# Performance work log

Hardware: AMD Instinct MI355X
Metric: run time of the kernel (lower is better)

The kernel has to match this reference:

```python
import jax, jax.numpy as jnp
import numpy as np

B, S, D, H = 2, 512, 512, 8
HD = D // H  # 64


def setup_inputs() -> dict:
    key = jax.random.key(0)
    ks = jax.random.split(key, 14)
    sd = 1.0 / np.sqrt(D)
    sh = 1.0 / np.sqrt(HD)
    return {
        "query": jax.random.normal(ks[0], (B, S, D), jnp.float32),
        "key_": jax.random.normal(ks[1], (B, S, D), jnp.float32),
        "value": jax.random.normal(ks[2], (B, S, D), jnp.float32),
        "Wq": jax.random.uniform(ks[3], (D, D), jnp.float32, -sd, sd),
        "bq": jax.random.uniform(ks[4], (D,), jnp.float32, -sd, sd),
        "Wk": jax.random.uniform(ks[5], (D, D), jnp.float32, -sd, sd),
        "bk": jax.random.uniform(ks[6], (D,), jnp.float32, -sd, sd),
        "Wv": jax.random.uniform(ks[7], (D, D), jnp.float32, -sd, sd),
        "bv": jax.random.uniform(ks[8], (D,), jnp.float32, -sd, sd),
        "Wo": jax.random.uniform(ks[9], (D, D), jnp.float32, -sd, sd),
        "bo": jax.random.uniform(ks[10], (D,), jnp.float32, -sd, sd),
        "Aq": jax.random.uniform(ks[11], (HD, HD), jnp.float32, -sh, sh),
        "Ak": jax.random.uniform(ks[12], (HD, HD), jnp.float32, -sh, sh),
        "av": jax.random.normal(ks[13], (HD,), jnp.float32) * sh,
    }


def _heads(x):
    b, s, _ = x.shape
    return x.reshape(b, s, H, HD).transpose(0, 2, 1, 3)  # [b,h,s,hd]


def reference(query, key_, value, Wq, bq, Wk, bk, Wv, bv, Wo, bo, Aq, Ak, av):
    q = _heads(query @ Wq + bq)   # [b,h,q,hd]
    k = _heads(key_ @ Wk + bk)    # [b,h,k,hd]
    v = _heads(value @ Wv + bv)   # [b,h,k,hd]
    # additive (Bahdanau-style) scores: tanh(add_q(q)[:,:,:,None]+add_k(k)[:,:,None]) . av
    q_term = (q @ Aq)[:, :, :, None, :]   # [b,h,q,1,hd]
    k_term = (k @ Ak)[:, :, None, :, :]   # [b,h,1,k,hd]
    scores = jnp.einsum('bhqkd,d->bhqk', jnp.tanh(q_term + k_term), av)
    attn_weights = jax.nn.softmax(scores, axis=-1)  # dropout is identity at eval
    ctx = jnp.einsum('bhqk,bhkd->bhqd', attn_weights, v)
    b, _, s, _ = ctx.shape
    ctx = ctx.transpose(0, 2, 1, 3).reshape(b, s, D)
    out = ctx @ Wo + bo
    return out, attn_weights
```

## Files before the change

kernel.cpp:

```cpp
#include <hip/hip_runtime.h>
#include <math.h>

#define Bb 2
#define Ss 512
#define Dd 512
#define Hh 8
#define HDd 64
#define BS (Bb*Ss)

#if __has_builtin(__builtin_amdgcn_exp2f)
#define EXP2F(x) __builtin_amdgcn_exp2f(x)
#else
#define EXP2F(x) exp2f(x)
#endif
#if __has_builtin(__builtin_amdgcn_rcpf)
#define RCPF(x) __builtin_amdgcn_rcpf(x)
#else
#define RCPF(x) (1.0f/(x))
#endif

typedef float v4f __attribute__((ext_vector_type(4)));
typedef short v8s __attribute__((ext_vector_type(8)));

struct HL { short h, l; };

__device__ __forceinline__ HL split1(float x) {
  unsigned u = __builtin_bit_cast(unsigned, x);
  unsigned h = (u + 0x7fffu + ((u >> 16) & 1u)) >> 16;
  float hf = __builtin_bit_cast(float, h << 16);
  float lo = x - hf;
  unsigned ul = __builtin_bit_cast(unsigned, lo);
  unsigned l = (ul + 0x7fffu + ((ul >> 16) & 1u)) >> 16;
  HL r; r.h = (short)h; r.l = (short)l;
  return r;
}

__device__ __forceinline__ void split8p(const float* __restrict__ xp, v8s& ah, v8s& al) {
#pragma unroll
  for (int j = 0; j < 8; j++) {
    const HL r = split1(xp[j]);
    ah[j] = r.h; al[j] = r.l;
  }
}

__device__ __forceinline__ void split8v(float4 x0, float4 x1, v8s& ah, v8s& al) {
  HL r;
  r = split1(x0.x); ah[0] = r.h; al[0] = r.l;
  r = split1(x0.y); ah[1] = r.h; al[1] = r.l;
  r = split1(x0.z); ah[2] = r.h; al[2] = r.l;
  r = split1(x0.w); ah[3] = r.h; al[3] = r.l;
  r = split1(x1.x); ah[4] = r.h; al[4] = r.l;
  r = split1(x1.y); ah[5] = r.h; al[5] = r.l;
  r = split1(x1.z); ah[6] = r.h; al[6] = r.l;
  r = split1(x1.w); ah[7] = r.h; al[7] = r.l;
}

__global__ __launch_bounds__(256) void qkv_all(
    const float* __restrict__ Xq, const float* __restrict__ Xk, const float* __restrict__ Xv,
    const float* __restrict__ Wq, const float* __restrict__ Wk, const float* __restrict__ Wv,
    const float* __restrict__ Wo,
    const float* __restrict__ bq, const float* __restrict__ bk, const float* __restrict__ bv,
    const float* __restrict__ Aq, const float* __restrict__ Ak,
    float* __restrict__ EQ, float* __restrict__ EKt, float* __restrict__ Vw,
    short* __restrict__ WoPk)
{
  __shared__ __align__(16) short fragH[2][4][64][8];
  __shared__ __align__(16) short fragL[2][4][64][8];
  __shared__ float qs[64][68];
  __shared__ float qs2[16][260];

  const int z = blockIdx.z;
  const float* X    = (z == 0) ? Xq : (z == 1) ? Xk : Xv;
  const float* W    = (z == 0) ? Wq : (z == 1) ? Wk : Wv;
  const float* bias = (z == 0) ? bq : (z == 1) ? bk : bv;
  const int tid = threadIdx.x, l = tid & 63, w = tid >> 6;
  const int lm = l & 15, lq = l >> 4;
  const int h = blockIdx.x;
  const int r0 = blockIdx.y * 64;

  v4f acc[4] = {{0.f,0.f,0.f,0.f},{0.f,0.f,0.f,0.f},{0.f,0.f,0.f,0.f},{0.f,0.f,0.f,0.f}};
  const float* xrow = X + (size_t)(r0 + w * 16 + lm) * Dd + lq * 8;

  for (int kt = 0; kt < 16; ++kt) {
    const int buf = kt & 1;
    const float4 xa0 = *(const float4*)&xrow[kt * 32];
    const float4 xa1 = *(const float4*)&xrow[kt * 32 + 4];
    {
      v8s hh, ll;
#pragma unroll
      for (int j = 0; j < 8; j++) {
        const float x = W[(size_t)(kt * 32 + lq * 8 + j) * Dd + h * 64 + w * 16 + lm];
        const HL r = split1(x);
        hh[j] = r.h; ll[j] = r.l;
      }
      *(v8s*)&fragH[buf][w][l][0] = hh;
      *(v8s*)&fragL[buf][w][l][0] = ll;
    }
    __syncthreads();
    v8s ah, al;
    split8v(xa0, xa1, ah, al);
#pragma unroll
    for (int t = 0; t < 4; t++) {
      const v8s bh = *(const v8s*)&fragH[buf][t][l][0];
      const v8s bl = *(const v8s*)&fragL[buf][t][l][0];
      acc[t] = __builtin_amdgcn_mfma_f32_16x16x32_bf16(ah, bh, acc[t], 0, 0, 0);
      acc[t] = __builtin_amdgcn_mfma_f32_16x16x32_bf16(ah, bl, acc[t], 0, 0, 0);
      acc[t] = __builtin_amdgcn_mfma_f32_16x16x32_bf16(al, bh, acc[t], 0, 0, 0);
    }
  }

  if (z == 2) {
#pragma unroll
    for (int t = 0; t < 4; t++) {
      const int n = h * 64 + t * 16 + lm;
      const float bvv = bias[n];
#pragma unroll
      for (int r = 0; r < 4; r++)
        Vw[(size_t)(r0 + w * 16 + lq * 4 + r) * Dd + n] = acc[t][r] + bvv;
    }
    {
      const int tau = (blockIdx.y * 8 + h) * 4 + w;
      const int nt = tau >> 4, kt = tau & 15;
      v8s hh, ll;
#pragma unroll
      for (int j = 0; j < 8; j++) {
        const float x = Wo[(size_t)(kt * 32 + lq * 8 + j) * Dd + nt * 16 + lm];
        const HL r = split1(x);
        hh[j] = r.h; ll[j] = r.l;
      }
      *(v8s*)&WoPk[((size_t)tau * 64 + l) * 16 + 0] = hh;
      *(v8s*)&WoPk[((size_t)tau * 64 + l) * 16 + 8] = ll;
    }
    return;
  }

#pragma unroll
  for (int t = 0; t < 4; t++) {
    const int n = h * 64 + t * 16 + lm;
    const float bvv = bias[n];
#pragma unroll
    for (int r = 0; r < 4; r++)
      qs[w * 16 + lq * 4 + r][t * 16 + lm] = acc[t][r] + bvv;
  }
  __syncthreads();

  const float* Am = (z == 0) ? Aq : Ak;
  v4f a2[4] = {{0.f,0.f,0.f,0.f},{0.f,0.f,0.f,0.f},{0.f,0.f,0.f,0.f},{0.f,0.f,0.f,0.f}};
#pragma unroll
  for (int kt2 = 0; kt2 < 2; ++kt2) {
    v8s ah, al;
    split8p(&qs[w * 16 + lm][kt2 * 32 + lq * 8], ah, al);
#pragma unroll
    for (int t2 = 0; t2 < 4; t2++) {
      v8s bh, bl;
#pragma unroll
      for (int j = 0; j < 8; j++) {
        const float x = Am[(kt2 * 32 + lq * 8 + j) * HDd + t2 * 16 + lm]
                        * 2.885390081777927f;
        const HL r = split1(x);
        bh[j] = r.h; bl[j] = r.l;
      }
      a2[t2] = __builtin_amdgcn_mfma_f32_16x16x32_bf16(ah, bh, a2[t2], 0, 0, 0);
      a2[t2] = __builtin_amdgcn_mfma_f32_16x16x32_bf16(ah, bl, a2[t2], 0, 0, 0);
      a2[t2] = __builtin_amdgcn_mfma_f32_16x16x32_bf16(al, bh, a2[t2], 0, 0, 0);
    }
  }

  if (z == 0) {
#pragma unroll
    for (int t2 = 0; t2 < 4; t2++)
#pragma unroll
      for (int rr = 0; rr < 4; rr++)
        EQ[(size_t)(r0 + w * 16 + lq * 4 + rr) * Dd + h * 64 + t2 * 16 + lm] = EXP2F(a2[t2][rr]);
  } else {
#pragma unroll
    for (int t2 = 0; t2 < 4; t2++)
#pragma unroll
      for (int rr = 0; rr < 4; rr++)
        qs2[4 * t2 + (lm >> 2)][(w * 16 + lq * 4 + rr) * 4 + (lm & 3)] = EXP2F(a2[t2][rr]);
    __syncthreads();
    const int b = r0 >> 9;
    const size_t base = (size_t)(b * 8 + h) * 16 * 2048 + (size_t)(r0 & 511) * 4;
#pragma unroll
    for (int i = 0; i < 4; i++) {
      const int f = i * 1024 + tid * 4;
      const int dt = f >> 8, c = f & 255;
      *(float4*)&EKt[base + (size_t)dt * 2048 + c] = *(const float4*)&qs2[dt][c];
    }
  }
}

__device__ __forceinline__ float grp4(v4f e, v4f ek, v4f av4) {
  const float A = __builtin_fmaf(e.x, ek.x, 1.f);
  const float B = __builtin_fmaf(e.y, ek.y, 1.f);
  const float C = __builtin_fmaf(e.z, ek.z, 1.f);
  const float D = __builtin_fmaf(e.w, ek.w, 1.f);
  const float AB = A * B;
  const float CD = C * D;
  const float n1 = __builtin_fmaf(av4.y, A, av4.x * B);
  const float n2 = __builtin_fmaf(av4.w, C, av4.z * D);
  const float N = __builtin_fmaf(n2, AB, n1 * CD);
  return N * RCPF(AB * CD);
}

__global__ __launch_bounds__(256, 6) void attn_kernel(
    const float* __restrict__ EQ, const float* __restrict__ EKt,
    const float* __restrict__ V, const float* __restrict__ av,
    float* __restrict__ attnW, float* __restrict__ CTX)
{
  __shared__ float uni[4128];
  __shared__ float eq_s[8][64];
  __shared__ float avn[64];
  float (*ekb)[2048] = (float (*)[2048])uni;

  const int tid = threadIdx.x, l = tid & 63, w = tid >> 6;
  const int q0 = blockIdx.x * 8;
  const int bh = blockIdx.y;
  const int b = bh >> 3, h = bh & 7;

  if (tid < 128) {
    const int f = tid * 4, r = f >> 6, d = f & 63;
    *(float4*)&eq_s[r][d] =
        *(const float4*)&EQ[(size_t)(b * Ss + q0 + r) * Dd + h * HDd + d];
  } else if (tid < 192) {
    avn[tid - 128] = -2.f * av[tid - 128];
  }

  const float* ekrow = EKt + (size_t)bh * 16 * 2048;
  {
    *(float4*)&ekb[0][tid * 4]        = *(const float4*)&ekrow[tid * 4];
    *(float4*)&ekb[0][1024 + tid * 4] = *(const float4*)&ekrow[1024 + tid * 4];
  }
  __syncthreads();

  const int qg = w * 2;
  float a[2][8];
#pragma unroll
  for (int j = 0; j < 2; j++)
#pragma unroll
    for (int kg = 0; kg < 8; kg++) a[j][kg] = 0.f;

#pragma unroll 1
  for (int dt = 0; dt < 16; ++dt) {
    const int cb = dt & 1, nb = cb ^ 1;
    const int dtn = (dt < 15) ? dt + 1 : 15;
    const float4 p0 = *(const float4*)&ekrow[(size_t)dtn * 2048 + tid * 4];
    const float4 p1 = *(const float4*)&ekrow[(size_t)dtn * 2048 + 1024 + tid * 4];

    const v4f av4 = *(const v4f*)&avn[dt * 4];
    const v4f e0 = *(const v4f*)&eq_s[qg + 0][dt * 4];
    const v4f e1 = *(const v4f*)&eq_s[qg + 1][dt * 4];
#pragma unroll
    for (int kg = 0; kg < 8; kg++) {
      const v4f ek = *(const v4f*)&ekb[cb][kg * 256 + l * 4];
      a[0][kg] += grp4(e0, ek, av4);
      a[1][kg] += grp4(e1, ek, av4);
    }
    *(float4*)&ekb[nb][tid * 4]        = p0;
    *(float4*)&ekb[nb][1024 + tid * 4] = p1;
    __syncthreads();
  }

#pragma unroll
  for (int j = 0; j < 2; j++) {
    float m = -1e30f;
#pragma unroll
    for (int kg = 0; kg < 8; kg++) m = fmaxf(m, a[j][kg]);
#pragma unroll
    for (int off = 32; off >= 1; off >>= 1) m = fmaxf(m, __shfl_xor(m, off, 64));
    float s = 0.f;
#pragma unroll
    for (int kg = 0; kg < 8; kg++) {
      a[j][kg] = EXP2F((a[j][kg] - m) * 1.4426950408889634f);
      s += a[j][kg];
    }
#pragma unroll
    for (int off = 32; off >= 1; off >>= 1) s += __shfl_xor(s, off, 64);
    const float inv = RCPF(s);
    float* arow = attnW + ((size_t)bh * Ss + q0 + qg + j) * Ss;
#pragma unroll
    for (int kg = 0; kg < 8; kg++) {
      const float wv = a[j][kg] * inv;
      uni[(qg + j) * 516 + kg * 64 + l] = wv;
      arow[kg * 64 + l] = wv;
    }
  }
  __syncthreads();

  {
    const int cq = tid >> 5;
    const int dq = (tid & 31) * 2;
    const float* vb = V + (size_t)b * Ss * Dd + h * HDd + dq;
    const float* scr = &uni[cq * 516];
    float ox = 0.f, oy = 0.f;
    for (int kk = 0; kk < Ss; kk += 2) {
      const float2 wv = *(const float2*)&scr[kk];
      const float2 v0 = *(const float2*)&vb[(size_t)kk * Dd];
      const float2 v1 = *(const float2*)&vb[(size_t)(kk + 1) * Dd];
      ox += wv.x * v0.x + wv.y * v1.x;
      oy += wv.x * v0.y + wv.y * v1.y;
    }
    float2 o; o.x = ox; o.y = oy;
    *(float2*)&CTX[(size_t)(b * Ss + q0 + cq) * Dd + h * HDd + dq] = o;
  }
}

__global__ __launch_bounds__(256) void out_pk(
    const float* __restrict__ CTX, const short* __restrict__ WoPk,
    const float* __restrict__ bo, float* __restrict__ out)
{
  const int tid = threadIdx.x;
  const int l = tid & 63, w = tid >> 6;
  const int lm = l & 15, lq = l >> 4;
  const int m0 = blockIdx.y * 64 + w * 16;
  const int nt0 = blockIdx.x * 4;

  v4f acc[4] = {{0.f,0.f,0.f,0.f},{0.f,0.f,0.f,0.f},{0.f,0.f,0.f,0.f},{0.f,0.f,0.f,0.f}};
  const float* xrow = CTX + (size_t)(m0 + lm) * Dd + lq * 8;

#pragma unroll 2
  for (int kt = 0; kt < 16; ++kt) {
    v8s ah, al;
    split8p(xrow + kt * 32, ah, al);
#pragma unroll
    for (int t = 0; t < 4; t++) {
      const int tau = (nt0 + t) * 16 + kt;
      const size_t bi = ((size_t)tau * 64 + l) * 16;
      const v8s bh = *(const v8s*)&WoPk[bi + 0];
      const v8s bl = *(const v8s*)&WoPk[bi + 8];
      acc[t] = __builtin_amdgcn_mfma_f32_16x16x32_bf16(ah, bh, acc[t], 0, 0, 0);
      acc[t] = __builtin_amdgcn_mfma_f32_16x16x32_bf16(ah, bl, acc[t], 0, 0, 0);
      acc[t] = __builtin_amdgcn_mfma_f32_16x16x32_bf16(al, bh, acc[t], 0, 0, 0);
    }
  }
#pragma unroll
  for (int t = 0; t < 4; t++) {
    const int n = (nt0 + t) * 16 + lm;
    const float bv = bo[n];
#pragma unroll
    for (int r = 0; r < 4; r++)
      out[(size_t)(m0 + lq * 4 + r) * Dd + n] = acc[t][r] + bv;
  }
}

extern "C" void kernel_launch(void* const* d_in, const int* in_sizes, int n_in,
                              void* d_out, int out_size, void* d_ws, size_t ws_size,
                              hipStream_t stream) {
  (void)in_sizes; (void)n_in; (void)out_size; (void)ws_size;
  const float* query = (const float*)d_in[0];
  const float* key_  = (const float*)d_in[1];
  const float* value = (const float*)d_in[2];
  const float* Wq    = (const float*)d_in[3];
  const float* bq    = (const float*)d_in[4];
  const float* Wk    = (const float*)d_in[5];
  const float* bk    = (const float*)d_in[6];
  const float* Wv    = (const float*)d_in[7];
  const float* bv    = (const float*)d_in[8];
  const float* Wo    = (const float*)d_in[9];
  const float* bo    = (const float*)d_in[10];
  const float* Aq    = (const float*)d_in[11];
  const float* Ak    = (const float*)d_in[12];
  const float* av    = (const float*)d_in[13];

  float* outp = (float*)d_out;
  float* attn = outp + (size_t)BS * Dd;

  float* ws  = (float*)d_ws;
  float* EQ  = ws;
  float* EKt = ws + (size_t)BS * Dd;
  float* Vw  = ws + 2 * (size_t)BS * Dd;
  float* CTX = ws + 3 * (size_t)BS * Dd;
  short* WoPk = (short*)(ws + 4 * (size_t)BS * Dd);

  qkv_all<<<dim3(8, 16, 3), 256, 0, stream>>>(query, key_, value,
      Wq, Wk, Wv, Wo, bq, bk, bv, Aq, Ak, EQ, EKt, Vw, WoPk);
  attn_kernel<<<dim3(64, 16), 256, 0, stream>>>(EQ, EKt, Vw, av, attn, CTX);
  out_pk<<<dim3(8, 16), 256, 0, stream>>>(CTX, WoPk, bo, outp);
}
```

Baseline: 194.8 us.

## Process 16 queries per attention block with larger EK chunks and wider PV loads

Each attention block now handles 16 query rows instead of 8, so each wave computes scores for 4 queries against each EK tile loaded into shared memory. The EK staging moves from 2 KB-per-step double buffering to 8 KB chunks covering four d-steps each, which cuts the number of barriers. The PV product uses float4 V loads per thread. In exchange, shared memory rises to about 64 KB per block, the launch-bounds occupancy hint is dropped, and the grid is halved to 512 blocks, which lowers occupancy and parallelism.

```diff
diff --git a/kernel.cpp b/kernel.cpp
--- a/kernel.cpp
+++ b/kernel.cpp
@@ -203,66 +203,81 @@
   return N * RCPF(AB * CD);
 }
 
-__global__ __launch_bounds__(256, 6) void attn_kernel(
+__global__ __launch_bounds__(256) void attn_kernel(
     const float* __restrict__ EQ, const float* __restrict__ EKt,
     const float* __restrict__ V, const float* __restrict__ av,
     float* __restrict__ attnW, float* __restrict__ CTX)
 {
-  __shared__ float uni[4128];
-  __shared__ float eq_s[8][64];
+  __shared__ float uni[16384];
+  __shared__ float eq_s[16][64];
   __shared__ float avn[64];
-  float (*ekb)[2048] = (float (*)[2048])uni;
 
   const int tid = threadIdx.x, l = tid & 63, w = tid >> 6;
-  const int q0 = blockIdx.x * 8;
+  const int q0 = blockIdx.x * 16;
   const int bh = blockIdx.y;
   const int b = bh >> 3, h = bh & 7;
 
-  if (tid < 128) {
+  {
     const int f = tid * 4, r = f >> 6, d = f & 63;
     *(float4*)&eq_s[r][d] =
         *(const float4*)&EQ[(size_t)(b * Ss + q0 + r) * Dd + h * HDd + d];
-  } else if (tid < 192) {
-    avn[tid - 128] = -2.f * av[tid - 128];
-  }
-
-  const float* ekrow = EKt + (size_t)bh * 16 * 2048;
+    if (tid < 64) avn[tid] = -2.f * av[tid];
+  }
+
+  const float* ekbase = EKt + (size_t)bh * 16 * 2048;
   {
-    *(float4*)&ekb[0][tid * 4]        = *(const float4*)&ekrow[tid * 4];
-    *(float4*)&ekb[0][1024 + tid * 4] = *(const float4*)&ekrow[1024 + tid * 4];
+    float4 pre[8];
+#pragma unroll
+    for (int j = 0; j < 8; j++)
+      pre[j] = *(const float4*)&ekbase[j * 1024 + tid * 4];
+#pragma unroll
+    for (int j = 0; j < 8; j++)
+      *(float4*)&uni[j * 1024 + tid * 4] = pre[j];
   }
   __syncthreads();
 
-  const int qg = w * 2;
-  float a[2][8];
-#pragma unroll
-  for (int j = 0; j < 2; j++)
+  const int qg = w * 4;
+  float a[4][8];
+#pragma unroll
+  for (int j = 0; j < 4; j++)
 #pragma unroll
     for (int kg = 0; kg < 8; kg++) a[j][kg] = 0.f;
 
 #pragma unroll 1
-  for (int dt = 0; dt < 16; ++dt) {
-    const int cb = dt & 1, nb = cb ^ 1;
-    const int dtn = (dt < 15) ? dt + 1 : 15;
-    const float4 p0 = *(const float4*)&ekrow[(size_t)dtn * 2048 + tid * 4];
-    const float4 p1 = *(const float4*)&ekrow[(size_t)dtn * 2048 + 1024 + tid * 4];
-
-    const v4f av4 = *(const v4f*)&avn[dt * 4];
-    const v4f e0 = *(const v4f*)&eq_s[qg + 0][dt * 4];
-    const v4f e1 = *(const v4f*)&eq_s[qg + 1][dt * 4];
-#pragma unroll
-    for (int kg = 0; kg < 8; kg++) {
-      const v4f ek = *(const v4f*)&ekb[cb][kg * 256 + l * 4];
-      a[0][kg] += grp4(e0, ek, av4);
-      a[1][kg] += grp4(e1, ek, av4);
-    }
-    *(float4*)&ekb[nb][tid * 4]        = p0;
-    *(float4*)&ekb[nb][1024 + tid * 4] = p1;
+  for (int ch = 0; ch < 4; ++ch) {
+    const int cb = (ch & 1) * 8192;
+    const int nb = ((ch + 1) & 1) * 8192;
+    const int chn = (ch < 3) ? ch + 1 : 3;
+    float4 pre[8];
+#pragma unroll
+    for (int j = 0; j < 8; j++)
+      pre[j] = *(const float4*)&ekbase[(size_t)chn * 8192 + j * 1024 + tid * 4];
+
+#pragma unroll
+    for (int s = 0; s < 4; ++s) {
+      const int dt = ch * 4 + s;
+      const v4f av4 = *(const v4f*)&avn[dt * 4];
+      const v4f e0 = *(const v4f*)&eq_s[qg + 0][dt * 4];
+      const v4f e1 = *(const v4f*)&eq_s[qg + 1][dt * 4];
+      const v4f e2 = *(const v4f*)&eq_s[qg + 2][dt * 4];
+      const v4f e3 = *(const v4f*)&eq_s[qg + 3][dt * 4];
+#pragma unroll
+      for (int kg = 0; kg < 8; kg++) {
+        const v4f ek = *(const v4f*)&uni[cb + s * 2048 + kg * 256 + l * 4];
+        a[0][kg] += grp4(e0, ek, av4);
+        a[1][kg] += grp4(e1, ek, av4);
+        a[2][kg] += grp4(e2, ek, av4);
+        a[3][kg] += grp4(e3, ek, av4);
+      }
+    }
+#pragma unroll
+    for (int j = 0; j < 8; j++)
+      *(float4*)&uni[nb + j * 1024 + tid * 4] = pre[j];
     __syncthreads();
   }
 
 #pragma unroll
-  for (int j = 0; j < 2; j++) {
+  for (int j = 0; j < 4; j++) {
     float m = -1e30f;
 #pragma unroll
     for (int kg = 0; kg < 8; kg++) m = fmaxf(m, a[j][kg]);
@@ -288,20 +303,18 @@
   __syncthreads();
 
   {
-    const int cq = tid >> 5;
-    const int dq = (tid & 31) * 2;
+    const int cq = tid >> 4;
+    const int dq = (tid & 15) * 4;
     const float* vb = V + (size_t)b * Ss * Dd + h * HDd + dq;
     const float* scr = &uni[cq * 516];
-    float ox = 0.f, oy = 0.f;
+    v4f o = {0.f, 0.f, 0.f, 0.f};
     for (int kk = 0; kk < Ss; kk += 2) {
       const float2 wv = *(const float2*)&scr[kk];
-      const float2 v0 = *(const float2*)&vb[(size_t)kk * Dd];
-      const float2 v1 = *(const float2*)&vb[(size_t)(kk + 1) * Dd];
-      ox += wv.x * v0.x + wv.y * v1.x;
-      oy += wv.x * v0.y + wv.y * v1.y;
-    }
-    float2 o; o.x = ox; o.y = oy;
-    *(float2*)&CTX[(size_t)(b * Ss + q0 + cq) * Dd + h * HDd + dq] = o;
+      const v4f v0 = *(const v4f*)&vb[(size_t)kk * Dd];
+      const v4f v1 = *(const v4f*)&vb[(size_t)(kk + 1) * Dd];
+      o += wv.x * v0 + wv.y * v1;
+    }
+    *(v4f*)&CTX[(size_t)(b * Ss + q0 + cq) * Dd + h * HDd + dq] = o;
   }
 }
 
@@ -374,6 +387,6 @@
 
   qkv_all<<<dim3(8, 16, 3), 256, 0, stream>>>(query, key_, value,
       Wq, Wk, Wv, Wo, bq, bk, bv, Aq, Ak, EQ, EKt, Vw, WoPk);
-  attn_kernel<<<dim3(64, 16), 256, 0, stream>>>(EQ, EKt, Vw, av, attn, CTX);
+  attn_kernel<<<dim3(32, 16), 256, 0, stream>>>(EQ, EKt, Vw, av, attn, CTX);
   out_pk<<<dim3(8, 16), 256, 0, stream>>>(CTX, WoPk, bo, outp);
 }
```

Measured after the change: 191.3 us. No clear change (-1.8%).
